# Performance work log

Hardware: AMD Instinct MI355X
Metric: run time of the kernel (lower is better)

## Reference

```python
import jax, jax.numpy as jnp
import numpy as np
from jax import lax

L, B, N_IN, N_OUT, K = 1024, 16, 1024, 512, 5


def setup_inputs() -> dict:
    key = jax.random.key(0)
    k0, k1, k2, k3, k4 = jax.random.split(key, 5)
    val_range = (6.0 / (N_IN + N_OUT)) ** 0.5
    x = jax.random.normal(k0, (L, B, N_IN), dtype=jnp.float32)
    weight = jax.random.uniform(k1, (N_IN, N_OUT * K), dtype=jnp.float32,
                                minval=-val_range, maxval=val_range)
    bias = jax.random.normal(k2, (N_OUT * K,), dtype=jnp.float32) * 0.1
    bias_eps = jax.random.normal(k3, (N_OUT,), dtype=jnp.float32) * 0.1
    bias_final = jax.random.normal(k4, (N_OUT * 2,), dtype=jnp.float32) * 0.1
    return {"x": x, "weight": weight, "bias": bias,
            "bias_eps": bias_eps, "bias_final": bias_final}


def reference(x, weight, bias, bias_eps, bias_final):
    # x: [L, B, n_in]; unidirectional (bidir=1), real semiring, output gate, tanh
    length, batch, n_in = x.shape
    n_out = N_OUT
    u_ = (x.reshape(-1, n_in) @ weight).reshape(length, batch, n_out, K)
    b = bias.reshape(K, n_out)  # [5, n_out]: in1, in2, f1, f2, out
    forget_bias1, forget_bias2, output_bias = b[2], b[3], b[4]
    output = jax.nn.sigmoid(u_[..., 4] + output_bias)      # [L, B, n_out]
    forget1 = jax.nn.sigmoid(u_[..., 2] + forget_bias1)
    forget2 = jax.nn.sigmoid(u_[..., 3] + forget_bias2)
    u1, u2 = u_[..., 0], u_[..., 1]
    eps = jax.nn.sigmoid(bias_eps)                          # [n_out]

    def step(carry, inp):
        c1_prev, c2_prev = carry
        f1t, f2t, u1t, u2t = inp
        c1_t = c1_prev * f1t + u1t
        c2_t = c2_prev * f2t + (eps + c1_prev) * u2t
        return (c1_t, c2_t), (c1_t, c2_t)

    init = (jnp.zeros((batch, n_out), x.dtype), jnp.zeros((batch, n_out), x.dtype))
    (c1_final, c2_final), (c1s, c2s) = lax.scan(step, init, (forget1, forget2, u1, u2))

    rho = jax.nn.sigmoid(bias_final.reshape(n_out, 2)) * 2.0
    cs = c1s * rho[:, 0] + c2s * rho[:, 1]
    gcs = jnp.tanh(output * cs)                             # [L, B, n_out]
    return gcs, c1_final, c2_final
```

## Files before the change

kernel.cpp:

```cpp
#include <hip/hip_runtime.h>
#include <cstdint>

#define LSEQ 1024
#define BATCH 16
#define NIN 1024
#define NOUT 512
#define KGATE 5
#define NCOL (NOUT * KGATE)
#define MTOT (LSEQ * BATCH)
#define CHAINS (BATCH * NOUT)
#define OUT_GCS (LSEQ * BATCH * NOUT)
#define SEG 32
#define SLEN 32
#define PLANE ((size_t)MTOT * NOUT)
#define SMP ((size_t)SEG * CHAINS)

#define BM 256
#define BN 128
#define BK 32
#define NT (NIN / BK)

typedef _Float16 f16x8 __attribute__((ext_vector_type(8)));
typedef _Float16 f16x4 __attribute__((ext_vector_type(4)));
typedef _Float16 f16x2 __attribute__((ext_vector_type(2)));
typedef float f32x4 __attribute__((ext_vector_type(4)));

__device__ __forceinline__ void async16(const void* g, void* l) {
    __builtin_amdgcn_global_load_lds(
        (const __attribute__((address_space(1))) void*)(uintptr_t)g,
        (__attribute__((address_space(3))) void*)(uintptr_t)l,
        16, 0, 0);
}

__device__ __forceinline__ float fsigmoid(float x) {
    return 1.0f / (1.0f + __expf(-x));
}

__global__ void convert_x_k(const float* __restrict__ x, _Float16* __restrict__ xb, int n8) {
    int i = blockIdx.x * blockDim.x + threadIdx.x;
    if (i < n8) {
        float4 a = ((const float4*)x)[2 * i];
        float4 b = ((const float4*)x)[2 * i + 1];
        f16x8 h;
        h[0] = (_Float16)a.x; h[1] = (_Float16)a.y; h[2] = (_Float16)a.z; h[3] = (_Float16)a.w;
        h[4] = (_Float16)b.x; h[5] = (_Float16)b.y; h[6] = (_Float16)b.z; h[7] = (_Float16)b.w;
        ((f16x8*)xb)[i] = h;
    }
}

__global__ __launch_bounds__(256) void transpose_w_k(const float* __restrict__ w, _Float16* __restrict__ wT) {
    __shared__ float lds[32][33];
    int t = threadIdx.x;
    int col = t & 31;
    int rowg = t >> 5;
    int n0 = blockIdx.x * 32;
    int k0 = blockIdx.y * 32;
#pragma unroll
    for (int i = 0; i < 4; i++) {
        int r = rowg + i * 8;
        lds[r][col] = w[(size_t)(k0 + r) * NCOL + n0 + col];
    }
    __syncthreads();
#pragma unroll
    for (int i = 0; i < 4; i++) {
        int r = rowg + i * 8;
        int c = n0 + r;
        int row = (c % 5) * NOUT + (c / 5);
        wT[(size_t)row * NIN + k0 + col] = (_Float16)lds[col][r];
    }
}

__global__ __launch_bounds__(256, 2) void gemm_gates_k(const _Float16* __restrict__ A,
                                                       const _Float16* __restrict__ BT,
                                                       const float* __restrict__ bias,
                                                       _Float16* __restrict__ planes) {
    __shared__ _Float16 lds[24576];
    const int t = threadIdx.x;
    const int w = t >> 6, lane = t & 63;
    const int q = lane >> 4, r16 = lane & 15;
    const int wm = (w >> 1) * 128, wn = (w & 1) * 64;
    const int m0 = blockIdx.x * BM, n0 = blockIdx.y * BN;

    const int swz = (q ^ ((r16 >> 1) & 3)) << 4;
    const int aBase = (wm + r16) * 64 + swz;
    const int bBase = 32768 + (wn + r16) * 64 + swz;

    const int rS = t >> 2;
    const int skS = (t & 3) ^ ((rS >> 1) & 3);
    const _Float16* aS = A + (size_t)(m0 + rS) * NIN + skS * 8;
    const _Float16* bS = BT + (size_t)(n0 + rS) * NIN + skS * 8;
    char* const ldsb = (char*)lds;
    const int aDst = t * 16;
    const int bDst = 32768 + t * 16;

    auto stage = [&](int tile, int nxt) {
        const _Float16* ap = aS + (size_t)tile * BK;
        const _Float16* bp = bS + (size_t)tile * BK;
#pragma unroll
        for (int L = 0; L < 4; L++)
            async16(ap + (size_t)L * 64 * NIN, ldsb + nxt * 16384 + aDst + L * 4096);
#pragma unroll
        for (int L = 0; L < 2; L++)
            async16(bp + (size_t)L * 64 * NIN, ldsb + nxt * 8192 + bDst + L * 4096);
    };

    f32x4 acc[8][4] = {};

    stage(0, 0);
    __syncthreads();

#pragma unroll 2
    for (int tt = 0; tt < NT; tt++) {
        const int cur = tt & 1;
        if (tt + 1 < NT) stage(tt + 1, cur ^ 1);

        f16x8 af[8], bf[4];
        const char* ab = ldsb + cur * 16384 + aBase;
        const char* bb = ldsb + cur * 8192 + bBase;
#pragma unroll
        for (int i = 0; i < 8; i++) af[i] = *(const f16x8*)(ab + i * 1024);
#pragma unroll
        for (int j = 0; j < 4; j++) bf[j] = *(const f16x8*)(bb + j * 1024);

        __builtin_amdgcn_s_setprio(1);
#pragma unroll
        for (int i = 0; i < 8; i++)
#pragma unroll
            for (int j = 0; j < 4; j++)
                acc[i][j] = __builtin_amdgcn_mfma_f32_16x16x32_f16(bf[j], af[i], acc[i][j], 0, 0, 0);
        __builtin_amdgcn_s_setprio(0);

        __syncthreads();
    }

    const int g = n0 >> 9;
    const int nb = n0 & (NOUT - 1);
    _Float16* plane = planes + (size_t)g * PLANE;
#pragma unroll
    for (int i = 0; i < 8; i++) {
        int m = m0 + wm + i * 16 + r16;
        _Float16* prow = plane + (size_t)m * NOUT + nb;
#pragma unroll
        for (int j = 0; j < 4; j++) {
            int nn = wn + j * 16 + q * 4;
            float4 bv = *(const float4*)(bias + n0 + nn);
            f16x4 hv;
#pragma unroll
            for (int reg = 0; reg < 4; reg++) {
                float v = acc[i][j][reg];
                float b = (reg == 0) ? bv.x : (reg == 1) ? bv.y : (reg == 2) ? bv.z : bv.w;
                if (g >= 2) v = fsigmoid(v + b);
                hv[reg] = (_Float16)v;
            }
            *(f16x4*)(prow + nn) = hv;
        }
    }
}

__global__ __launch_bounds__(256) void compose_k(const _Float16* __restrict__ planes,
                                                 const float* __restrict__ beps,
                                                 float* __restrict__ SM) {
    int u = blockIdx.x * 256 + threadIdx.x;
    int t2 = u & (CHAINS / 2 - 1);
    int s = u >> 12;
    int tch = t2 << 1;
    int n = tch & (NOUT - 1);
    float eps[2] = { fsigmoid(beps[n]), fsigmoid(beps[n + 1]) };
    float a11[2] = {1.0f, 1.0f}, a21[2] = {}, a22[2] = {1.0f, 1.0f}, b1[2] = {}, b2[2] = {};
    const f16x2* p2 = (const f16x2*)planes;
    const size_t P2E = PLANE >> 1;
    const size_t estep = CHAINS >> 1;
    size_t e = ((size_t)(s * SLEN) * CHAINS + tch) >> 1;
    f16x2 u1n = p2[e], u2n = p2[P2E + e], f1n = p2[2 * P2E + e], f2n = p2[3 * P2E + e];
#pragma unroll 4
    for (int j = 0; j < SLEN; j++) {
        f16x2 u1c = u1n, u2c = u2n, f1c = f1n, f2c = f2n;
        if (j + 1 < SLEN) {
            e += estep;
            u1n = p2[e]; u2n = p2[P2E + e]; f1n = p2[2 * P2E + e]; f2n = p2[3 * P2E + e];
        }
#pragma unroll
        for (int c = 0; c < 2; c++) {
            float u1 = (float)u1c[c], u2 = (float)u2c[c];
            float f1 = (float)f1c[c], f2 = (float)f2c[c];
            float na11 = f1 * a11[c];
            float na21 = fmaf(u2, a11[c], f2 * a21[c]);
            float na22 = f2 * a22[c];
            float nb1  = fmaf(f1, b1[c], u1);
            float nb2  = fmaf(u2, b1[c], fmaf(f2, b2[c], eps[c] * u2));
            a11[c] = na11; a21[c] = na21; a22[c] = na22; b1[c] = nb1; b2[c] = nb2;
        }
    }
    size_t idx = (size_t)s * CHAINS + tch;
    *(float2*)(SM + idx)           = make_float2(a11[0], a11[1]);
    *(float2*)(SM + SMP + idx)     = make_float2(a21[0], a21[1]);
    *(float2*)(SM + 2 * SMP + idx) = make_float2(a22[0], a22[1]);
    *(float2*)(SM + 3 * SMP + idx) = make_float2(b1[0], b1[1]);
    *(float2*)(SM + 4 * SMP + idx) = make_float2(b2[0], b2[1]);
}

__global__ __launch_bounds__(256) void segscan_k(const float* __restrict__ SM,
                                                 float* __restrict__ segc,
                                                 float* __restrict__ out) {
    int t = blockIdx.x * 256 + threadIdx.x;
    float c1 = 0.0f, c2 = 0.0f;
    float a11n = SM[t], a21n = SM[SMP + t], a22n = SM[2 * SMP + t];
    float b1n = SM[3 * SMP + t], b2n = SM[4 * SMP + t];
#pragma unroll
    for (int s = 0; s < SEG; s++) {
        float a11 = a11n, a21 = a21n, a22 = a22n, b1 = b1n, b2 = b2n;
        if (s + 1 < SEG) {
            size_t nx = (size_t)(s + 1) * CHAINS + t;
            a11n = SM[nx]; a21n = SM[SMP + nx]; a22n = SM[2 * SMP + nx];
            b1n = SM[3 * SMP + nx]; b2n = SM[4 * SMP + nx];
        }
        size_t idx = (size_t)s * CHAINS + t;
        segc[idx] = c1;
        segc[SMP + idx] = c2;
        float c1n = fmaf(a11, c1, b1);
        float c2n = fmaf(a21, c1, fmaf(a22, c2, b2));
        c1 = c1n; c2 = c2n;
    }
    out[OUT_GCS + t] = c1;
    out[OUT_GCS + CHAINS + t] = c2;
}

__global__ __launch_bounds__(256) void apply_k(const _Float16* __restrict__ planes,
                                               const float* __restrict__ segc,
                                               const float* __restrict__ beps,
                                               const float* __restrict__ bfin,
                                               float* __restrict__ out) {
    int u = blockIdx.x * 256 + threadIdx.x;
    int t2 = u & (CHAINS / 2 - 1);
    int s = u >> 12;
    int tch = t2 << 1;
    int n = tch & (NOUT - 1);
    float eps[2], rho0[2], rho1[2], c1[2], c2[2];
#pragma unroll
    for (int c = 0; c < 2; c++) {
        eps[c]  = fsigmoid(beps[n + c]);
        rho0[c] = 2.0f * fsigmoid(bfin[2 * (n + c)]);
        rho1[c] = 2.0f * fsigmoid(bfin[2 * (n + c) + 1]);
    }
    size_t idx = (size_t)s * CHAINS + tch;
    float2 c1v = *(const float2*)(segc + idx);
    float2 c2v = *(const float2*)(segc + SMP + idx);
    c1[0] = c1v.x; c1[1] = c1v.y; c2[0] = c2v.x; c2[1] = c2v.y;
    const f16x2* p2 = (const f16x2*)planes;
    const size_t P2E = PLANE >> 1;
    const size_t estep = CHAINS >> 1;
    size_t e2 = ((size_t)(s * SLEN) * CHAINS + tch) >> 1;
    size_t eo = (size_t)(s * SLEN) * CHAINS + tch;
    f16x2 u1n = p2[e2], u2n = p2[P2E + e2], f1n = p2[2 * P2E + e2],
          f2n = p2[3 * P2E + e2], on = p2[4 * P2E + e2];
#pragma unroll 4
    for (int j = 0; j < SLEN; j++) {
        f16x2 u1c = u1n, u2c = u2n, f1c = f1n, f2c = f2n, oc = on;
        if (j + 1 < SLEN) {
            e2 += estep;
            u1n = p2[e2]; u2n = p2[P2E + e2]; f1n = p2[2 * P2E + e2];
            f2n = p2[3 * P2E + e2]; on = p2[4 * P2E + e2];
        }
        float yr[2];
#pragma unroll
        for (int c = 0; c < 2; c++) {
            float u1 = (float)u1c[c], u2 = (float)u2c[c];
            float f1 = (float)f1c[c], f2 = (float)f2c[c];
            float o  = (float)oc[c];
            float c1p = c1[c];
            c1[c] = fmaf(c1p, f1, u1);
            c2[c] = fmaf(c2[c], f2, (eps[c] + c1p) * u2);
            float cs = fmaf(c1[c], rho0[c], c2[c] * rho1[c]);
            float y = o * cs;
            y = fminf(9.0f, fmaxf(-9.0f, y));
            float ex = __expf(2.0f * y);
            yr[c] = (ex - 1.0f) / (ex + 1.0f);
        }
        *(float2*)(out + eo) = make_float2(yr[0], yr[1]);
        eo += CHAINS;
    }
}

extern "C" void kernel_launch(void* const* d_in, const int* in_sizes, int n_in,
                              void* d_out, int out_size, void* d_ws, size_t ws_size,
                              hipStream_t stream) {
    const float* x    = (const float*)d_in[0];
    const float* wgt  = (const float*)d_in[1];
    const float* bias = (const float*)d_in[2];
    const float* beps = (const float*)d_in[3];
    const float* bfin = (const float*)d_in[4];
    float* out = (float*)d_out;

    char* p = (char*)d_ws;
    _Float16* wT     = (_Float16*)p; p += (size_t)NCOL * NIN * 2;
    _Float16* xb     = (_Float16*)p; p += (size_t)MTOT * NIN * 2;
    _Float16* planes = (_Float16*)p; p += 5 * PLANE * 2;
    float* SM        = (float*)p;    p += 5 * SMP * 4;
    float* segc      = (float*)p;    p += 2 * SMP * 4;

    transpose_w_k<<<dim3(NCOL / 32, NIN / 32), 256, 0, stream>>>(wgt, wT);

    int n8 = MTOT * NIN / 8;
    convert_x_k<<<dim3((n8 + 255) / 256), 256, 0, stream>>>(x, xb, n8);

    gemm_gates_k<<<dim3(MTOT / BM, NCOL / BN), 256, 0, stream>>>(xb, wT, bias, planes);

    compose_k<<<dim3(SEG * CHAINS / 2 / 256), 256, 0, stream>>>(planes, beps, SM);
    segscan_k<<<dim3(CHAINS / 256), 256, 0, stream>>>(SM, segc, out);
    apply_k<<<dim3(SEG * CHAINS / 2 / 256), 256, 0, stream>>>(planes, segc, beps, bfin, out);
}
```

Before: 272.4 us.

## Stage gate planes through LDS in compose and apply kernels with one chain per thread

The compose and apply scan kernels now load each 8-timestep chunk of the gate planes with wide 16-byte coalesced loads into a double-buffered LDS tile. Each thread then reads its own chain column from shared memory instead of doing strided 4-byte global loads. Each thread now handles one chain instead of two, which doubles the block count and adds parallelism. The cost is block barriers, LDS traffic, and scalar 4-byte output stores replacing the float2 stores.

```diff
diff --git a/kernel.cpp b/kernel.cpp
--- a/kernel.cpp
+++ b/kernel.cpp
@@ -20,9 +20,11 @@
 #define BK 32
 #define NT (NIN / BK)
 
+#define CGRP 256
+#define JPH 8
+
 typedef _Float16 f16x8 __attribute__((ext_vector_type(8)));
 typedef _Float16 f16x4 __attribute__((ext_vector_type(4)));
-typedef _Float16 f16x2 __attribute__((ext_vector_type(2)));
 typedef float f32x4 __attribute__((ext_vector_type(4)));
 
 __device__ __forceinline__ void async16(const void* g, void* l) {
@@ -160,43 +162,64 @@
 __global__ __launch_bounds__(256) void compose_k(const _Float16* __restrict__ planes,
                                                  const float* __restrict__ beps,
                                                  float* __restrict__ SM) {
-    int u = blockIdx.x * 256 + threadIdx.x;
-    int t2 = u & (CHAINS / 2 - 1);
-    int s = u >> 12;
-    int tch = t2 << 1;
-    int n = tch & (NOUT - 1);
-    float eps[2] = { fsigmoid(beps[n]), fsigmoid(beps[n + 1]) };
-    float a11[2] = {1.0f, 1.0f}, a21[2] = {}, a22[2] = {1.0f, 1.0f}, b1[2] = {}, b2[2] = {};
-    const f16x2* p2 = (const f16x2*)planes;
-    const size_t P2E = PLANE >> 1;
-    const size_t estep = CHAINS >> 1;
-    size_t e = ((size_t)(s * SLEN) * CHAINS + tch) >> 1;
-    f16x2 u1n = p2[e], u2n = p2[P2E + e], f1n = p2[2 * P2E + e], f2n = p2[3 * P2E + e];
-#pragma unroll 4
-    for (int j = 0; j < SLEN; j++) {
-        f16x2 u1c = u1n, u2c = u2n, f1c = f1n, f2c = f2n;
-        if (j + 1 < SLEN) {
-            e += estep;
-            u1n = p2[e]; u2n = p2[P2E + e]; f1n = p2[2 * P2E + e]; f2n = p2[3 * P2E + e];
+    __shared__ _Float16 tile[2][4][JPH][CGRP];
+    const int t = threadIdx.x;
+    const int s = blockIdx.x >> 5;
+    const int grp = blockIdx.x & 31;
+    const int tch = grp * CGRP + t;
+    const int n = tch & (NOUT - 1);
+    const int jl = t >> 5, ci = t & 31;
+
+    auto stage = [&](int ph, int b) {
+        const int j0 = s * SLEN + ph * JPH;
+        f16x8 v[4];
+#pragma unroll
+        for (int r = 0; r < 4; r++)
+            v[r] = *(const f16x8*)(planes + (size_t)r * PLANE + (size_t)(j0 + jl) * CHAINS + grp * CGRP + ci * 8);
+#pragma unroll
+        for (int r = 0; r < 4; r++)
+            *(f16x8*)((char*)tile + b * 16384 + (t + r * 256) * 16) = v[r];
+    };
+
+    float eps = fsigmoid(beps[n]);
+    float a11 = 1.0f, a21 = 0.0f, a22 = 1.0f, b1 = 0.0f, b2 = 0.0f;
+
+    auto computeph = [&](int b) {
+#pragma unroll
+        for (int j = 0; j < JPH; j++) {
+            float u1 = (float)tile[b][0][j][t];
+            float u2 = (float)tile[b][1][j][t];
+            float f1 = (float)tile[b][2][j][t];
+            float f2 = (float)tile[b][3][j][t];
+            float na11 = f1 * a11;
+            float na21 = fmaf(u2, a11, f2 * a21);
+            float na22 = f2 * a22;
+            float nb1  = fmaf(f1, b1, u1);
+            float nb2  = fmaf(u2, b1, fmaf(f2, b2, eps * u2));
+            a11 = na11; a21 = na21; a22 = na22; b1 = nb1; b2 = nb2;
         }
-#pragma unroll
-        for (int c = 0; c < 2; c++) {
-            float u1 = (float)u1c[c], u2 = (float)u2c[c];
-            float f1 = (float)f1c[c], f2 = (float)f2c[c];
-            float na11 = f1 * a11[c];
-            float na21 = fmaf(u2, a11[c], f2 * a21[c]);
-            float na22 = f2 * a22[c];
-            float nb1  = fmaf(f1, b1[c], u1);
-            float nb2  = fmaf(u2, b1[c], fmaf(f2, b2[c], eps[c] * u2));
-            a11[c] = na11; a21[c] = na21; a22[c] = na22; b1[c] = nb1; b2[c] = nb2;
-        }
-    }
+    };
+
+    stage(0, 0);
+    stage(1, 1);
+    __syncthreads();
+    computeph(0);
+    __syncthreads();
+    stage(2, 0);
+    __syncthreads();
+    computeph(1);
+    __syncthreads();
+    stage(3, 1);
+    __syncthreads();
+    computeph(0);
+    computeph(1);
+
     size_t idx = (size_t)s * CHAINS + tch;
-    *(float2*)(SM + idx)           = make_float2(a11[0], a11[1]);
-    *(float2*)(SM + SMP + idx)     = make_float2(a21[0], a21[1]);
-    *(float2*)(SM + 2 * SMP + idx) = make_float2(a22[0], a22[1]);
-    *(float2*)(SM + 3 * SMP + idx) = make_float2(b1[0], b1[1]);
-    *(float2*)(SM + 4 * SMP + idx) = make_float2(b2[0], b2[1]);
+    SM[idx]           = a11;
+    SM[SMP + idx]     = a21;
+    SM[2 * SMP + idx] = a22;
+    SM[3 * SMP + idx] = b1;
+    SM[4 * SMP + idx] = b2;
 }
 
 __global__ __launch_bounds__(256) void segscan_k(const float* __restrict__ SM,
@@ -230,55 +253,66 @@
                                                const float* __restrict__ beps,
                                                const float* __restrict__ bfin,
                                                float* __restrict__ out) {
-    int u = blockIdx.x * 256 + threadIdx.x;
-    int t2 = u & (CHAINS / 2 - 1);
-    int s = u >> 12;
-    int tch = t2 << 1;
-    int n = tch & (NOUT - 1);
-    float eps[2], rho0[2], rho1[2], c1[2], c2[2];
-#pragma unroll
-    for (int c = 0; c < 2; c++) {
-        eps[c]  = fsigmoid(beps[n + c]);
-        rho0[c] = 2.0f * fsigmoid(bfin[2 * (n + c)]);
-        rho1[c] = 2.0f * fsigmoid(bfin[2 * (n + c) + 1]);
-    }
+    __shared__ _Float16 tile[2][5][JPH][CGRP];
+    const int t = threadIdx.x;
+    const int s = blockIdx.x >> 5;
+    const int grp = blockIdx.x & 31;
+    const int tch = grp * CGRP + t;
+    const int n = tch & (NOUT - 1);
+    const int jl = t >> 5, ci = t & 31;
+
+    auto stage = [&](int ph, int b) {
+        const int j0 = s * SLEN + ph * JPH;
+        f16x8 v[5];
+#pragma unroll
+        for (int r = 0; r < 5; r++)
+            v[r] = *(const f16x8*)(planes + (size_t)r * PLANE + (size_t)(j0 + jl) * CHAINS + grp * CGRP + ci * 8);
+#pragma unroll
+        for (int r = 0; r < 5; r++)
+            *(f16x8*)((char*)tile + b * 20480 + (t + r * 256) * 16) = v[r];
+    };
+
     size_t idx = (size_t)s * CHAINS + tch;
-    float2 c1v = *(const float2*)(segc + idx);
-    float2 c2v = *(const float2*)(segc + SMP + idx);
-    c1[0] = c1v.x; c1[1] = c1v.y; c2[0] = c2v.x; c2[1] = c2v.y;
-    const f16x2* p2 = (const f16x2*)planes;
-    const size_t P2E = PLANE >> 1;
-    const size_t estep = CHAINS >> 1;
-    size_t e2 = ((size_t)(s * SLEN) * CHAINS + tch) >> 1;
-    size_t eo = (size_t)(s * SLEN) * CHAINS + tch;
-    f16x2 u1n = p2[e2], u2n = p2[P2E + e2], f1n = p2[2 * P2E + e2],
-          f2n = p2[3 * P2E + e2], on = p2[4 * P2E + e2];
-#pragma unroll 4
-    for (int j = 0; j < SLEN; j++) {
-        f16x2 u1c = u1n, u2c = u2n, f1c = f1n, f2c = f2n, oc = on;
-        if (j + 1 < SLEN) {
-            e2 += estep;
-            u1n = p2[e2]; u2n = p2[P2E + e2]; f1n = p2[2 * P2E + e2];
-            f2n = p2[3 * P2E + e2]; on = p2[4 * P2E + e2];
-        }
-        float yr[2];
-#pragma unroll
-        for (int c = 0; c < 2; c++) {
-            float u1 = (float)u1c[c], u2 = (float)u2c[c];
-            float f1 = (float)f1c[c], f2 = (float)f2c[c];
-            float o  = (float)oc[c];
-            float c1p = c1[c];
-            c1[c] = fmaf(c1p, f1, u1);
-            c2[c] = fmaf(c2[c], f2, (eps[c] + c1p) * u2);
-            float cs = fmaf(c1[c], rho0[c], c2[c] * rho1[c]);
+    float c1 = segc[idx];
+    float c2 = segc[SMP + idx];
+    float eps  = fsigmoid(beps[n]);
+    float rho0 = 2.0f * fsigmoid(bfin[2 * n]);
+    float rho1 = 2.0f * fsigmoid(bfin[2 * n + 1]);
+
+    auto computeph = [&](int ph, int b) {
+        size_t eo = (size_t)(s * SLEN + ph * JPH) * CHAINS + tch;
+#pragma unroll
+        for (int j = 0; j < JPH; j++) {
+            float u1 = (float)tile[b][0][j][t];
+            float u2 = (float)tile[b][1][j][t];
+            float f1 = (float)tile[b][2][j][t];
+            float f2 = (float)tile[b][3][j][t];
+            float o  = (float)tile[b][4][j][t];
+            float c1p = c1;
+            c1 = fmaf(c1p, f1, u1);
+            c2 = fmaf(c2, f2, (eps + c1p) * u2);
+            float cs = fmaf(c1, rho0, c2 * rho1);
             float y = o * cs;
             y = fminf(9.0f, fmaxf(-9.0f, y));
             float ex = __expf(2.0f * y);
-            yr[c] = (ex - 1.0f) / (ex + 1.0f);
+            out[eo] = (ex - 1.0f) / (ex + 1.0f);
+            eo += CHAINS;
         }
-        *(float2*)(out + eo) = make_float2(yr[0], yr[1]);
-        eo += CHAINS;
-    }
+    };
+
+    stage(0, 0);
+    stage(1, 1);
+    __syncthreads();
+    computeph(0, 0);
+    __syncthreads();
+    stage(2, 0);
+    __syncthreads();
+    computeph(1, 1);
+    __syncthreads();
+    stage(3, 1);
+    __syncthreads();
+    computeph(2, 0);
+    computeph(3, 1);
 }
 
 extern "C" void kernel_launch(void* const* d_in, const int* in_sizes, int n_in,
@@ -305,7 +339,7 @@
 
     gemm_gates_k<<<dim3(MTOT / BM, NCOL / BN), 256, 0, stream>>>(xb, wT, bias, planes);
 
-    compose_k<<<dim3(SEG * CHAINS / 2 / 256), 256, 0, stream>>>(planes, beps, SM);
+    compose_k<<<dim3(SEG * (CHAINS / CGRP)), 256, 0, stream>>>(planes, beps, SM);
     segscan_k<<<dim3(CHAINS / 256), 256, 0, stream>>>(SM, segc, out);
-    apply_k<<<dim3(SEG * CHAINS / 2 / 256), 256, 0, stream>>>(planes, segc, beps, bfin, out);
-}
+    apply_k<<<dim3(SEG * (CHAINS / CGRP)), 256, 0, stream>>>(planes, segc, beps, bfin, out);
+}
```

Measured after the change: 269.5 us. No clear change (-1.1%).
